# Kernel tuning notes

Hardware: AMD Instinct MI355X
Metric: run time of the kernel (lower is better)

The kernel has to match this reference:

```python
import jax, jax.numpy as jnp
import numpy as np
from jax import lax

B, S, T = 32, 64, 64
E, H = 256, 512
VS, VT = 32000, 32000


def lstm_layer(x, h0, c0, Wih, Whh, b):
    """Single-layer LSTM, batch_first. x: [B,T,in], h0/c0: [B,H].
    Gate order matches PyTorch: i, f, g, o. b = b_ih + b_hh ([4H]).
    Returns (outputs [B,T,H], hT [B,H], cT [B,H])."""
    xW = jnp.einsum('bti,gi->btg', x, Wih) + b  # precompute input projection [B,T,4H]

    def step(carry, xw_t):
        h, c = carry
        gates = xw_t + h @ Whh.T
        i, f, g, o = jnp.split(gates, 4, axis=-1)
        c = jax.nn.sigmoid(f) * c + jax.nn.sigmoid(i) * jnp.tanh(g)
        h = jax.nn.sigmoid(o) * jnp.tanh(c)
        return (h, c), h

    (hT, cT), hs = lax.scan(step, (h0, c0), jnp.swapaxes(xW, 0, 1))
    return jnp.swapaxes(hs, 0, 1), hT, cT


def setup_inputs() -> dict:
    key = jax.random.key(0)
    ks = jax.random.split(key, 24)
    w = lambda k, shape: (0.02 * jax.random.normal(k, shape)).astype(jnp.float32)
    inp = {
        'src': jax.random.randint(ks[0], (B, S), 0, VS),
        'tgt': jax.random.randint(ks[1], (B, T), 0, VT),
        'enc_emb': w(ks[2], (VS, E)),
        'dec_emb': w(ks[3], (VT, E)),
        # encoder LSTM (2 layers, unidirectional)
        'enc_Wih0': w(ks[4], (4 * H, E)),
        'enc_Whh0': w(ks[5], (4 * H, H)),
        'enc_b0': jnp.zeros((4 * H,), jnp.float32),
        'enc_Wih1': w(ks[6], (4 * H, H)),
        'enc_Whh1': w(ks[7], (4 * H, H)),
        'enc_b1': jnp.zeros((4 * H,), jnp.float32),
        # decoder LSTM (2 layers), input = embed + context -> E + H
        'dec_Wih0': w(ks[8], (4 * H, E + H)),
        'dec_Whh0': w(ks[9], (4 * H, H)),
        'dec_b0': jnp.zeros((4 * H,), jnp.float32),
        'dec_Wih1': w(ks[10], (4 * H, H)),
        'dec_Whh1': w(ks[11], (4 * H, H)),
        'dec_b1': jnp.zeros((4 * H,), jnp.float32),
        # output projection: Linear(H,H) -> tanh -> Linear(H,VT)
        'proj_W1': w(ks[12], (H, H)),
        'proj_b1': jnp.zeros((H,), jnp.float32),
        'proj_W2': w(ks[13], (VT, H)),
        'proj_b2': jnp.zeros((VT,), jnp.float32),
    }
    return inp


def reference(src, tgt, enc_emb, dec_emb,
              enc_Wih0, enc_Whh0, enc_b0, enc_Wih1, enc_Whh1, enc_b1,
              dec_Wih0, dec_Whh0, dec_b0, dec_Wih1, dec_Whh1, dec_b1,
              proj_W1, proj_b1, proj_W2, proj_b2):
    z = jnp.zeros((src.shape[0], H), jnp.float32)
    # --- encode ---
    xe = enc_emb[src]                                        # [B,S,E]
    e0, h0, c0 = lstm_layer(xe, z, z, enc_Wih0, enc_Whh0, enc_b0)
    e1, h1, c1 = lstm_layer(e0, z, z, enc_Wih1, enc_Whh1, enc_b1)
    # constant context = mean over encoder outputs (recomputed per-step in torch, hoisted here)
    context = e1.mean(axis=1)                                # [B,H]
    # --- decode with teacher forcing: input at step t is tgt[:, t] ---
    xd = dec_emb[tgt]                                        # [B,T,E]
    ctx = jnp.broadcast_to(context[:, None, :], (xd.shape[0], xd.shape[1], H))
    rnn_in = jnp.concatenate([xd, ctx], axis=-1)             # [B,T,E+H]
    d0, _, _ = lstm_layer(rnn_in, h0, c0, dec_Wih0, dec_Whh0, dec_b0)
    d1, _, _ = lstm_layer(d0, h1, c1, dec_Wih1, dec_Whh1, dec_b1)
    # --- output projection ---
    hid = jnp.tanh(d1 @ proj_W1.T + proj_b1)                 # [B,T,H]
    logits = hid @ proj_W2.T + proj_b2                       # [B,T,VT]
    return logits
```

## Files before the change

### kernel.cpp

```cpp
#include <hip/hip_runtime.h>

typedef unsigned short ushort_t;
typedef __attribute__((ext_vector_type(8))) short bf16x8;
typedef __attribute__((ext_vector_type(4))) float f32x4;

#define BB 32
#define TT 64
#define HH 512
#define G4H 2048

__device__ __forceinline__ ushort_t f2bf(float f) {
    unsigned int u = __float_as_uint(f);
    unsigned int r = (u + 0x7fffu + ((u >> 16) & 1u)) >> 16;
    return (ushort_t)r;
}
__device__ __forceinline__ float sigf(float x) { return 1.f / (1.f + __expf(-x)); }
__device__ __forceinline__ float tanh_(float x) {
    float e = __expf(2.f * x);
    return 1.f - 2.f / (e + 1.f);
}

__global__ void zero_init(float* zeros) {
    int t = threadIdx.x;
    if (t < 128) ((float4*)zeros)[t] = make_float4(0.f, 0.f, 0.f, 0.f);
}

__global__ void gather_rows(const int* __restrict__ idx, const float* __restrict__ emb,
                            float* __restrict__ out) {
    int row = blockIdx.x;
    int t = threadIdx.x;
    int id = idx[row];
    float4 v = *(const float4*)(emb + (size_t)id * 256 + t * 4);
    *(float4*)(out + (size_t)row * 256 + t * 4) = v;
}

__global__ __launch_bounds__(256) void gemm_f32(
    const float* __restrict__ A, int lda,
    const float* __restrict__ B, int ldb,
    const float* __restrict__ bias,
    void* __restrict__ Cv, int ldc,
    int M, int N, int K, int mode)
{
    __shared__ float As[16 * 68];
    __shared__ float Bs[16 * 68];
    const int tid = threadIdx.x;
    const int bm = blockIdx.y * 64, bn = blockIdx.x * 64;
    const int lr = tid >> 2, lk = (tid & 3) << 2;
    const int tr = (tid >> 4) << 2, tc = (tid & 15) << 2;
    float acc[4][4] = {};
    const int arow = bm + lr, brow = bn + lr;
    const bool aval = arow < M, bval = brow < N;
    const float* Ap = A + (size_t)arow * lda + lk;
    const float* Bp = B + (size_t)brow * ldb + lk;

    for (int k0 = 0; k0 < K; k0 += 16) {
        float4 av = make_float4(0.f, 0.f, 0.f, 0.f);
        float4 bv = make_float4(0.f, 0.f, 0.f, 0.f);
        if (aval) av = *(const float4*)(Ap + k0);
        if (bval) bv = *(const float4*)(Bp + k0);
        As[(lk + 0) * 68 + lr] = av.x; As[(lk + 1) * 68 + lr] = av.y;
        As[(lk + 2) * 68 + lr] = av.z; As[(lk + 3) * 68 + lr] = av.w;
        Bs[(lk + 0) * 68 + lr] = bv.x; Bs[(lk + 1) * 68 + lr] = bv.y;
        Bs[(lk + 2) * 68 + lr] = bv.z; Bs[(lk + 3) * 68 + lr] = bv.w;
        __syncthreads();
        #pragma unroll
        for (int kk = 0; kk < 16; kk++) {
            float4 a = *(const float4*)&As[kk * 68 + tr];
            float4 b = *(const float4*)&Bs[kk * 68 + tc];
            float ar[4] = {a.x, a.y, a.z, a.w};
            float br[4] = {b.x, b.y, b.z, b.w};
            #pragma unroll
            for (int i = 0; i < 4; i++)
                #pragma unroll
                for (int j = 0; j < 4; j++)
                    acc[i][j] = fmaf(ar[i], br[j], acc[i][j]);
        }
        __syncthreads();
    }
    #pragma unroll
    for (int i = 0; i < 4; i++) {
        int m = bm + tr + i;
        if (m >= M) continue;
        #pragma unroll
        for (int j = 0; j < 4; j++) {
            int n = bn + tc + j;
            if (n >= N) continue;
            float v = acc[i][j] + (bias ? bias[n] : 0.f);
            if (mode == 0) ((float*)Cv)[(size_t)m * ldc + n] = v;
            else ((ushort_t*)Cv)[(size_t)m * ldc + n] = f2bf(tanh_(v));
        }
    }
}

__global__ __launch_bounds__(256) void gemm_mfma(
    const float* __restrict__ A, int lda,
    const float* __restrict__ B, int ldb,
    const float* __restrict__ bias,
    void* __restrict__ Cv, int ldc, int K, int mode)
{
    __shared__ ushort_t As[128 * 72];
    __shared__ ushort_t Bs[128 * 72];
    const int tid = threadIdx.x;
    const int bm = blockIdx.x * 128, bn = blockIdx.y * 128;
    const int lane = tid & 63, wave = tid >> 6;
    const int wm = (wave & 1) * 64, wn = (wave >> 1) * 64;
    const int lr = lane & 15, lk = (lane >> 4) * 8;
    const int srow = tid >> 3, sch = tid & 7;
    f32x4 acc[4][4] = {};

    for (int k0 = 0; k0 < K; k0 += 64) {
        #pragma unroll
        for (int rr = 0; rr < 4; rr++) {
            int row = srow + rr * 32;
            const float* as = A + (size_t)(bm + row) * lda + k0 + sch * 8;
            float4 a0 = *(const float4*)as;
            float4 a1 = *(const float4*)(as + 4);
            int4 pa;
            pa.x = (int)f2bf(a0.x) | ((int)f2bf(a0.y) << 16);
            pa.y = (int)f2bf(a0.z) | ((int)f2bf(a0.w) << 16);
            pa.z = (int)f2bf(a1.x) | ((int)f2bf(a1.y) << 16);
            pa.w = (int)f2bf(a1.z) | ((int)f2bf(a1.w) << 16);
            *(int4*)&As[row * 72 + sch * 8] = pa;
            const float* bs = B + (size_t)(bn + row) * ldb + k0 + sch * 8;
            float4 f0 = *(const float4*)bs;
            float4 f1 = *(const float4*)(bs + 4);
            int4 pk;
            pk.x = (int)f2bf(f0.x) | ((int)f2bf(f0.y) << 16);
            pk.y = (int)f2bf(f0.z) | ((int)f2bf(f0.w) << 16);
            pk.z = (int)f2bf(f1.x) | ((int)f2bf(f1.y) << 16);
            pk.w = (int)f2bf(f1.z) | ((int)f2bf(f1.w) << 16);
            *(int4*)&Bs[row * 72 + sch * 8] = pk;
        }
        __syncthreads();
        #pragma unroll
        for (int k2 = 0; k2 < 64; k2 += 32) {
            bf16x8 a[4], bfr[4];
            #pragma unroll
            for (int i = 0; i < 4; i++)
                a[i] = *(const bf16x8*)&As[(wm + i * 16 + lr) * 72 + k2 + lk];
            #pragma unroll
            for (int j = 0; j < 4; j++)
                bfr[j] = *(const bf16x8*)&Bs[(wn + j * 16 + lr) * 72 + k2 + lk];
            #pragma unroll
            for (int i = 0; i < 4; i++)
                #pragma unroll
                for (int j = 0; j < 4; j++)
                    acc[i][j] = __builtin_amdgcn_mfma_f32_16x16x32_bf16(a[i], bfr[j], acc[i][j], 0, 0, 0);
        }
        __syncthreads();
    }
    const int r0 = (lane >> 4) * 4;
    #pragma unroll
    for (int j = 0; j < 4; j++) {
        int col = bn + wn + j * 16 + lr;
        float bv = bias ? bias[col] : 0.f;
        #pragma unroll
        for (int i = 0; i < 4; i++) {
            int row = bm + wm + i * 16 + r0;
            #pragma unroll
            for (int q = 0; q < 4; q++) {
                float v = acc[i][j][q] + bv;
                if (mode == 0) ((float*)Cv)[(size_t)(row + q) * ldc + col] = v;
                else ((ushort_t*)Cv)[(size_t)(row + q) * ldc + col] = f2bf(tanh_(v));
            }
        }
    }
}

__global__ void mean_ctx(const float* __restrict__ e1, float* __restrict__ ctx) {
    int g = blockIdx.x * 256 + threadIdx.x;
    int b = g >> 9, u = g & 511;
    float s = 0.f;
    #pragma unroll 8
    for (int t = 0; t < TT; t++) s += e1[((size_t)b * TT + t) * HH + u];
    ctx[g] = s * (1.f / 64.f);
}

#define LOADS16                                                            \
        "global_load_dwordx2 %0, %16, off sc0 sc1\n\t"                     \
        "global_load_dwordx2 %1, %16, off offset:256 sc0 sc1\n\t"          \
        "global_load_dwordx2 %2, %16, off offset:512 sc0 sc1\n\t"          \
        "global_load_dwordx2 %3, %16, off offset:768 sc0 sc1\n\t"          \
        "global_load_dwordx2 %4, %16, off offset:1024 sc0 sc1\n\t"         \
        "global_load_dwordx2 %5, %16, off offset:1280 sc0 sc1\n\t"         \
        "global_load_dwordx2 %6, %16, off offset:1536 sc0 sc1\n\t"         \
        "global_load_dwordx2 %7, %16, off offset:1792 sc0 sc1\n\t"         \
        "global_load_dwordx2 %8, %16, off offset:2048 sc0 sc1\n\t"         \
        "global_load_dwordx2 %9, %16, off offset:2304 sc0 sc1\n\t"         \
        "global_load_dwordx2 %10, %16, off offset:2560 sc0 sc1\n\t"        \
        "global_load_dwordx2 %11, %16, off offset:2816 sc0 sc1\n\t"        \
        "global_load_dwordx2 %12, %16, off offset:3072 sc0 sc1\n\t"        \
        "global_load_dwordx2 %13, %16, off offset:3328 sc0 sc1\n\t"        \
        "global_load_dwordx2 %14, %16, off offset:3584 sc0 sc1\n\t"        \
        "global_load_dwordx2 %15, %16, off offset:3840 sc0 sc1\n\t"

#define OUTS16(a) "=&v"(a[0]), "=&v"(a[1]), "=&v"(a[2]), "=&v"(a[3]),      \
                  "=&v"(a[4]), "=&v"(a[5]), "=&v"(a[6]), "=&v"(a[7]),      \
                  "=&v"(a[8]), "=&v"(a[9]), "=&v"(a[10]), "=&v"(a[11]),    \
                  "=&v"(a[12]), "=&v"(a[13]), "=&v"(a[14]), "=&v"(a[15])

__device__ __forceinline__ bool tag_ok16(const uint2* q, unsigned int tag) {
    unsigned int a = 0xFFFFFFFFu, o = 0u;
    #pragma unroll
    for (int i = 0; i < 16; i++) { a &= q[i].x & q[i].y; o |= q[i].x | q[i].y; }
    return ((a >> 16) == tag) & ((o >> 16) == tag);
}

__device__ __forceinline__ void poll16_f32(const uint2* rp, unsigned int tag, float* hd) {
    uint2 q[16];
    bool ok;
    do {
        asm volatile(LOADS16 "s_waitcnt vmcnt(0)"
                     : OUTS16(q) : "v"(rp) : "memory");
        __builtin_amdgcn_sched_barrier(0);
        ok = tag_ok16(q, tag);
    } while (!ok);
    #pragma unroll
    for (int i = 0; i < 16; i++)
        hd[32 * i] = __uint_as_float((q[i].x << 16) | (q[i].y & 0xFFFFu));
}
__device__ __forceinline__ void poll16_bf16(const uint2* rp, unsigned int tag, ushort_t* hd) {
    uint2 q[16];
    bool ok;
    do {
        asm volatile(LOADS16 "s_waitcnt vmcnt(0)"
                     : OUTS16(q) : "v"(rp) : "memory");
        __builtin_amdgcn_sched_barrier(0);
        ok = tag_ok16(q, tag);
    } while (!ok);
    #pragma unroll
    for (int i = 0; i < 16; i++)
        hd[32 * i] = f2bf(__uint_as_float((q[i].x << 16) | (q[i].y & 0xFFFFu)));
}
__device__ __forceinline__ void poll_dual(const uint2* rp1, unsigned int tag1, float* hd,
                                          const uint2* rp0, unsigned int tag0, ushort_t* ad) {
    uint2 q[16], r[16];
    bool ok;
    do {
        asm volatile(LOADS16 : OUTS16(q) : "v"(rp1) : "memory");
        asm volatile(LOADS16 "s_waitcnt vmcnt(0)"
                     : OUTS16(r) : "v"(rp0) : "memory");
        __builtin_amdgcn_sched_barrier(0);
        ok = tag_ok16(q, tag1) & tag_ok16(r, tag0);
    } while (!ok);
    #pragma unroll
    for (int i = 0; i < 16; i++) {
        hd[32 * i] = __uint_as_float((q[i].x << 16) | (q[i].y & 0xFFFFu));
        ad[32 * i] = f2bf(__uint_as_float((r[i].x << 16) | (r[i].y & 0xFFFFu)));
    }
}

__global__ __launch_bounds__(512) void scan_pair2(
    const float* __restrict__ gatesX0,
    const float* __restrict__ ctxAdd0,
    const float* __restrict__ Whh0,
    const float* __restrict__ Wih1,
    const float* __restrict__ Whh1,
    const float* __restrict__ b1,
    const float* __restrict__ h00, int sh00, const float* __restrict__ c00, int sc00,
    const float* __restrict__ h01, int sh01, const float* __restrict__ c01, int sc01,
    float* __restrict__ out0, float* __restrict__ out1,
    float* __restrict__ cT0o, float* __restrict__ cT1o,
    uint2* __restrict__ ring0, uint2* __restrict__ ring1,
    int tb0, int tb1)
{
    __shared__ float wlds[32 * 516];
    __shared__ float hmain[16 * 516];
    __shared__ float glds[16 * 36];
    __shared__ ushort_t ah[16 * 520];
    __shared__ float pglds[8 * 256];
    const int tid = threadIdx.x;
    const bool isL1 = blockIdx.x >= 128;
    const int rb = blockIdx.x & 127;
    const int bg = rb >> 6, ub = rb & 63, u0 = ub * 8;
    const int w = tid >> 6, l = tid & 63;
    const int bb = l >> 2, rr = w * 4 + (l & 3);
    const int grow = (rr >> 3) * HH + u0 + (rr & 7);
    const int batch = bg * 16 + bb;
    const int srow = tid >> 5, hc0 = tid & 31;

    {
        const float* W = isL1 ? Whh1 : Whh0;
        const int sr = tid >> 4, ch = (tid & 15) * 32;
        const float* ws = W + (size_t)((sr >> 3) * HH + u0 + (sr & 7)) * HH + ch;
        float* wd = &wlds[sr * 516 + ch];
        #pragma unroll
        for (int j = 0; j < 32; j += 4) *(f32x4*)(wd + j) = *(const f32x4*)(ws + j);
    }
    const int ni = w & 1, kh = w >> 1, lr = l & 15, ls = l >> 4;
    bf16x8 bfrag[4];
    if (isL1) {
        const int nrow = ni * 16 + lr;
        const int gN = (nrow >> 3) * HH + u0 + (nrow & 7);
        const float* wr = Wih1 + (size_t)gN * HH + kh * 128 + ls * 8;
        #pragma unroll
        for (int kk = 0; kk < 4; kk++) {
            float f[8];
            *(f32x4*)&f[0] = *(const f32x4*)(wr + kk * 32);
            *(f32x4*)&f[4] = *(const f32x4*)(wr + kk * 32 + 4);
            bf16x8 hv;
            #pragma unroll
            for (int j = 0; j < 8; j++) hv[j] = (short)f2bf(f[j]);
            bfrag[kk] = hv;
        }
    }
    {
        const float* hsrc = isL1 ? h01 : h00;
        const int hstr = isL1 ? sh01 : sh00;
        const float* hs = hsrc + (size_t)(bg * 16 + srow) * hstr;
        float* hd = &hmain[srow * 516 + hc0];
        #pragma unroll
        for (int j = 0; j < 16; j++) hd[32 * j] = hs[hc0 + 32 * j];
    }
    const int pb = tid >> 3, pu = tid & 7, gbatch = bg * 16 + pb;
    float creg = 0.f, b1v0 = 0.f, b1v1 = 0.f, b1v2 = 0.f, b1v3 = 0.f;
    if (tid < 128) {
        const float* ci = isL1 ? c01 : c00;
        const int cs = isL1 ? sc01 : sc00;
        creg = ci[(size_t)gbatch * cs + u0 + pu];
        if (isL1) {
            b1v0 = b1[0 * HH + u0 + pu]; b1v1 = b1[1 * HH + u0 + pu];
            b1v2 = b1[2 * HH + u0 + pu]; b1v3 = b1[3 * HH + u0 + pu];
        }
    }
    float xctx = 0.f, gx_cur = 0.f, gx_nxt = 0.f;
    const float* gxp = nullptr;
    if (!isL1) {
        gxp = gatesX0 + (size_t)batch * TT * G4H + grow;
        gx_cur = gxp[0];
        if (ctxAdd0) xctx = ctxAdd0[(size_t)batch * G4H + grow];
    } else {
        const uint2* rp = ring0 + ((size_t)0 * BB + bg * 16 + srow) * HH + hc0;
        poll16_bf16(rp, (unsigned int)(tb0 + 1), &ah[srow * 520 + hc0]);
    }
    float* outp = isL1 ? out1 : out0;
    uint2* ringp = isL1 ? ring1 : ring0;
    const int tbase = isL1 ? tb1 : tb0;

    for (int t = 0; t < TT; ++t) {
        __syncthreads();
        if (!isL1) {
            int tn = (t + 1 < TT) ? t + 1 : t;
            gx_nxt = gxp[(size_t)tn * G4H];
            f32x4 s = {0.f, 0.f, 0.f, 0.f};
            const float* hp = &hmain[bb * 516];
            const float* wp = &wlds[rr * 516];
            #pragma unroll 8
            for (int k = 0; k < HH; k += 4) {
                f32x4 hv = *(const f32x4*)(hp + k);
                f32x4 wv = *(const f32x4*)(wp + k);
                s.x = fmaf(hv.x, wv.x, s.x); s.y = fmaf(hv.y, wv.y, s.y);
                s.z = fmaf(hv.z, wv.z, s.z); s.w = fmaf(hv.w, wv.w, s.w);
            }
            glds[bb * 36 + rr] = gx_cur + xctx + ((s.x + s.y) + (s.z + s.w));
        } else {
            f32x4 acc = {0.f, 0.f, 0.f, 0.f};
            const ushort_t* ab = &ah[lr * 520 + kh * 128 + ls * 8];
            #pragma unroll
            for (int kk = 0; kk < 4; kk++) {
                bf16x8 av = *(const bf16x8*)(ab + kk * 32);
                acc = __builtin_amdgcn_mfma_f32_16x16x32_bf16(av, bfrag[kk], acc, 0, 0, 0);
            }
            #pragma unroll
            for (int q = 0; q < 4; q++)
                pglds[(kh * 2 + ni) * 256 + (ls * 4 + q) * 16 + lr] = acc[q];
            f32x4 s = {0.f, 0.f, 0.f, 0.f};
            const float* hp = &hmain[bb * 516];
            const float* wp = &wlds[rr * 516];
            #pragma unroll 8
            for (int k = 0; k < HH; k += 4) {
                f32x4 hv = *(const f32x4*)(hp + k);
                f32x4 wv = *(const f32x4*)(wp + k);
                s.x = fmaf(hv.x, wv.x, s.x); s.y = fmaf(hv.y, wv.y, s.y);
                s.z = fmaf(hv.z, wv.z, s.z); s.w = fmaf(hv.w, wv.w, s.w);
            }
            glds[bb * 36 + rr] = (s.x + s.y) + (s.z + s.w);
        }
        __syncthreads();
        const unsigned int tag = (unsigned int)(tbase + t + 1);
        if (tid < 128) {
            float pre[4];
            if (!isL1) {
                #pragma unroll
                for (int g = 0; g < 4; g++) pre[g] = glds[pb * 36 + g * 8 + pu];
            } else {
                float bv[4] = {b1v0, b1v1, b1v2, b1v3};
                #pragma unroll
                for (int g = 0; g < 4; g++) {
                    int r = g * 8 + pu;
                    int nit = r >> 4, cr = r & 15;
                    float p = glds[pb * 36 + r] + bv[g];
                    #pragma unroll
                    for (int k2 = 0; k2 < 4; k2++)
                        p += pglds[(k2 * 2 + nit) * 256 + pb * 16 + cr];
                    pre[g] = p;
                }
            }
            float c = sigf(pre[1]) * creg + sigf(pre[0]) * tanh_(pre[2]);
            float h = sigf(pre[3]) * tanh_(c);
            creg = c;
            outp[((size_t)gbatch * TT + t) * HH + u0 + pu] = h;
            unsigned int hu = __float_as_uint(h);
            uint2 wv2;
            wv2.x = (tag << 16) | (hu >> 16);
            wv2.y = (tag << 16) | (hu & 0xFFFFu);
            uint2* pp = ringp + ((size_t)t * BB + gbatch) * HH + u0 + pu;
            asm volatile("global_store_dwordx2 %0, %1, off sc0 sc1"
                         :: "v"(pp), "v"(wv2) : "memory");
            if (t == TT - 1) {
                if (!isL1 && cT0o) cT0o[(size_t)gbatch * HH + u0 + pu] = c;
                if (isL1 && cT1o)  cT1o[(size_t)gbatch * HH + u0 + pu] = c;
            }
        }
        if (t + 1 < TT) {
            if (!isL1) {
                const uint2* rp = ring0 + ((size_t)t * BB + bg * 16 + srow) * HH + hc0;
                poll16_f32(rp, tag, &hmain[srow * 516 + hc0]);
            } else {
                const uint2* rp1 = ring1 + ((size_t)t * BB + bg * 16 + srow) * HH + hc0;
                const uint2* rp0 = ring0 + ((size_t)(t + 1) * BB + bg * 16 + srow) * HH + hc0;
                poll_dual(rp1, tag, &hmain[srow * 516 + hc0],
                          rp0, (unsigned int)(tb0 + t + 2), &ah[srow * 520 + hc0]);
            }
        }
        gx_cur = gx_nxt;
    }
}

__global__ __launch_bounds__(256) void gemm_bf16(
    const ushort_t* __restrict__ A,
    const float* __restrict__ B,
    const float* __restrict__ bias,
    float* __restrict__ C, int M, int N, int K)
{
    __shared__ ushort_t As[128 * 72];
    __shared__ ushort_t Bs[128 * 72];
    const int tid = threadIdx.x;
    const int bm = blockIdx.x * 128, bn = blockIdx.y * 128;
    const int lane = tid & 63, wave = tid >> 6;
    const int wm = (wave & 1) * 64, wn = (wave >> 1) * 64;
    const int lr = lane & 15, lk = (lane >> 4) * 8;
    const int srow = tid >> 3, sch = tid & 7;
    f32x4 acc[4][4] = {};

    for (int k0 = 0; k0 < K; k0 += 64) {
        #pragma unroll
        for (int rr = 0; rr < 4; rr++) {
            int row = srow + rr * 32;
            const ushort_t* as = A + (size_t)(bm + row) * K + k0 + sch * 8;
            *(int4*)&As[row * 72 + sch * 8] = *(const int4*)as;
            const float* bs = B + (size_t)(bn + row) * K + k0 + sch * 8;
            float4 f0 = *(const float4*)bs;
            float4 f1 = *(const float4*)(bs + 4);
            int4 pk;
            pk.x = (int)f2bf(f0.x) | ((int)f2bf(f0.y) << 16);
            pk.y = (int)f2bf(f0.z) | ((int)f2bf(f0.w) << 16);
            pk.z = (int)f2bf(f1.x) | ((int)f2bf(f1.y) << 16);
            pk.w = (int)f2bf(f1.z) | ((int)f2bf(f1.w) << 16);
            *(int4*)&Bs[row * 72 + sch * 8] = pk;
        }
        __syncthreads();
        #pragma unroll
        for (int k2 = 0; k2 < 64; k2 += 32) {
            bf16x8 a[4], bfr[4];
            #pragma unroll
            for (int i = 0; i < 4; i++)
                a[i] = *(const bf16x8*)&As[(wm + i * 16 + lr) * 72 + k2 + lk];
            #pragma unroll
            for (int j = 0; j < 4; j++)
                bfr[j] = *(const bf16x8*)&Bs[(wn + j * 16 + lr) * 72 + k2 + lk];
            #pragma unroll
            for (int i = 0; i < 4; i++)
                #pragma unroll
                for (int j = 0; j < 4; j++)
                    acc[i][j] = __builtin_amdgcn_mfma_f32_16x16x32_bf16(a[i], bfr[j], acc[i][j], 0, 0, 0);
        }
        __syncthreads();
    }
    const int r0 = (lane >> 4) * 4;
    #pragma unroll
    for (int j = 0; j < 4; j++) {
        int col = bn + wn + j * 16 + lr;
        float bv = bias[col];
        #pragma unroll
        for (int i = 0; i < 4; i++) {
            int row = bm + wm + i * 16 + r0;
            #pragma unroll
            for (int q = 0; q < 4; q++)
                C[(size_t)(row + q) * N + col] = acc[i][j][q] + bv;
        }
    }
}

extern "C" void kernel_launch(void* const* d_in, const int* in_sizes, int n_in,
                              void* d_out, int out_size, void* d_ws, size_t ws_size,
                              hipStream_t stream) {
    const int*   src      = (const int*)d_in[0];
    const int*   tgt      = (const int*)d_in[1];
    const float* enc_emb  = (const float*)d_in[2];
    const float* dec_emb  = (const float*)d_in[3];
    const float* eWih0    = (const float*)d_in[4];
    const float* eWhh0    = (const float*)d_in[5];
    const float* eb0      = (const float*)d_in[6];
    const float* eWih1    = (const float*)d_in[7];
    const float* eWhh1    = (const float*)d_in[8];
    const float* eb1      = (const float*)d_in[9];
    const float* dWih0    = (const float*)d_in[10];
    const float* dWhh0    = (const float*)d_in[11];
    const float* db0      = (const float*)d_in[12];
    const float* dWih1    = (const float*)d_in[13];
    const float* dWhh1    = (const float*)d_in[14];
    const float* db1      = (const float*)d_in[15];
    const float* pW1      = (const float*)d_in[16];
    const float* pb1      = (const float*)d_in[17];
    const float* pW2      = (const float*)d_in[18];
    const float* pb2      = (const float*)d_in[19];
    float* out = (float*)d_out;

    float* fws   = (float*)d_ws;
    float* zeros = fws;
    float* cT0   = fws + 2048;
    float* cT1   = cT0 + 16384;
    float* ctx   = cT1 + 16384;
    float* ctxW  = ctx + 16384;
    ushort_t* hid = (ushort_t*)(ctxW + 65536);

    float* G0  = out;
    float* G1  = G0 + 4194304;
    float* G2  = G1 + 4194304;
    float* G3  = G2 + 4194304;
    float* xe  = G3 + 4194304;
    float* xd  = xe + 524288;
    float* e0  = xd + 524288;
    float* e1  = e0 + 1048576;
    float* d0  = e1 + 1048576;
    float* d1v = d0 + 1048576;
    uint2* ring0 = (uint2*)(d1v + 1048576);
    uint2* ring1 = ring0 + 1048576;

    zero_init<<<1, 256, 0, stream>>>(zeros);
    gather_rows<<<2048, 64, 0, stream>>>(src, enc_emb, xe);
    gather_rows<<<2048, 64, 0, stream>>>(tgt, dec_emb, xd);

    gemm_mfma<<<dim3(16, 16), 256, 0, stream>>>(xe, 256, eWih0, 256, eb0, G0, 2048, 256, 0);
    gemm_mfma<<<dim3(16, 16), 256, 0, stream>>>(xd, 256, dWih0, 768, db0, G2, 2048, 256, 0);

    scan_pair2<<<256, 512, 0, stream>>>(
        G0, nullptr, eWhh0, eWih1, eWhh1, eb1,
        zeros, 0, zeros, 0, zeros, 0, zeros, 0,
        e0, e1, cT0, cT1, ring0, ring1, 0, 64);

    mean_ctx<<<64, 256, 0, stream>>>(e1, ctx);
    gemm_f32<<<dim3(32, 1), 256, 0, stream>>>(ctx, 512, dWih0 + 256, 768, nullptr, ctxW, 2048, 32, 2048, 512, 0);

    scan_pair2<<<256, 512, 0, stream>>>(
        G2, ctxW, dWhh0, dWih1, dWhh1, db1,
        e0 + 63 * 512, 64 * 512, cT0, 512,
        e1 + 63 * 512, 64 * 512, cT1, 512,
        d0, d1v, nullptr, nullptr, ring0, ring1, 128, 192);

    gemm_mfma<<<dim3(16, 4), 256, 0, stream>>>(d1v, 512, pW1, 512, pb1, hid, 512, 512, 2);
    gemm_bf16<<<dim3(16, 250), 256, 0, stream>>>(hid, pW2, pb2, out, 2048, 32000, 512);
}
```

Baseline: 1.737 ms.

## Compute layer-1 recurrent matmul with split-bf16 MFMA instead of fp32 FMA

In the layer-1 scan blocks, the fp32 h·Whh1 dot-product loop is replaced by bf16 MFMA using a hi/lo split of both h and Whh1 (three MFMAs per k-slice), folded into the same accumulator as the Wih1 projection. Whh1 fragments now live in registers rather than LDS, and the hidden state is stored as hi/lo bf16 arrays. The aim is to shorten the serial per-step recurrent compute on the critical path. The cost is extra MFMAs, register pressure and split conversions, and the ring polling changes from one combined dual poll to two sequential polls.

```diff
diff --git a/kernel.cpp b/kernel.cpp
--- a/kernel.cpp
+++ b/kernel.cpp
@@ -13,6 +13,12 @@
     unsigned int u = __float_as_uint(f);
     unsigned int r = (u + 0x7fffu + ((u >> 16) & 1u)) >> 16;
     return (ushort_t)r;
+}
+__device__ __forceinline__ void split_bf(float f, ushort_t& hi, ushort_t& lo) {
+    unsigned int hu = f2bf(f);
+    hi = (ushort_t)hu;
+    float hf = __uint_as_float((unsigned int)hu << 16);
+    lo = f2bf(f - hf);
 }
 __device__ __forceinline__ float sigf(float x) { return 1.f / (1.f + __expf(-x)); }
 __device__ __forceinline__ float tanh_(float x) {
@@ -232,21 +238,21 @@
     for (int i = 0; i < 16; i++)
         hd[32 * i] = f2bf(__uint_as_float((q[i].x << 16) | (q[i].y & 0xFFFFu)));
 }
-__device__ __forceinline__ void poll_dual(const uint2* rp1, unsigned int tag1, float* hd,
-                                          const uint2* rp0, unsigned int tag0, ushort_t* ad) {
-    uint2 q[16], r[16];
+__device__ __forceinline__ void poll16_hilo(const uint2* rp, unsigned int tag,
+                                            ushort_t* hh, ushort_t* hl) {
+    uint2 q[16];
     bool ok;
     do {
-        asm volatile(LOADS16 : OUTS16(q) : "v"(rp1) : "memory");
         asm volatile(LOADS16 "s_waitcnt vmcnt(0)"
-                     : OUTS16(r) : "v"(rp0) : "memory");
+                     : OUTS16(q) : "v"(rp) : "memory");
         __builtin_amdgcn_sched_barrier(0);
-        ok = tag_ok16(q, tag1) & tag_ok16(r, tag0);
+        ok = tag_ok16(q, tag);
     } while (!ok);
     #pragma unroll
     for (int i = 0; i < 16; i++) {
-        hd[32 * i] = __uint_as_float((q[i].x << 16) | (q[i].y & 0xFFFFu));
-        ad[32 * i] = f2bf(__uint_as_float((r[i].x << 16) | (r[i].y & 0xFFFFu)));
+        float v = __uint_as_float((q[i].x << 16) | (q[i].y & 0xFFFFu));
+        ushort_t hi, lo; split_bf(v, hi, lo);
+        hh[32 * i] = hi; hl[32 * i] = lo;
     }
 }
 
@@ -268,6 +274,8 @@
     __shared__ float hmain[16 * 516];
     __shared__ float glds[16 * 36];
     __shared__ ushort_t ah[16 * 520];
+    __shared__ ushort_t ahh[16 * 520];
+    __shared__ ushort_t ahl[16 * 520];
     __shared__ float pglds[8 * 256];
     const int tid = threadIdx.x;
     const bool isL1 = blockIdx.x >= 128;
@@ -279,20 +287,20 @@
     const int batch = bg * 16 + bb;
     const int srow = tid >> 5, hc0 = tid & 31;
 
-    {
-        const float* W = isL1 ? Whh1 : Whh0;
+    if (!isL1) {
         const int sr = tid >> 4, ch = (tid & 15) * 32;
-        const float* ws = W + (size_t)((sr >> 3) * HH + u0 + (sr & 7)) * HH + ch;
+        const float* ws = Whh0 + (size_t)((sr >> 3) * HH + u0 + (sr & 7)) * HH + ch;
         float* wd = &wlds[sr * 516 + ch];
         #pragma unroll
         for (int j = 0; j < 32; j += 4) *(f32x4*)(wd + j) = *(const f32x4*)(ws + j);
     }
     const int ni = w & 1, kh = w >> 1, lr = l & 15, ls = l >> 4;
-    bf16x8 bfrag[4];
+    bf16x8 bfrag[4], wh_hi[4], wh_lo[4];
     if (isL1) {
         const int nrow = ni * 16 + lr;
         const int gN = (nrow >> 3) * HH + u0 + (nrow & 7);
         const float* wr = Wih1 + (size_t)gN * HH + kh * 128 + ls * 8;
+        const float* wr2 = Whh1 + (size_t)gN * HH + kh * 128 + ls * 8;
         #pragma unroll
         for (int kk = 0; kk < 4; kk++) {
             float f[8];
@@ -302,15 +310,33 @@
             #pragma unroll
             for (int j = 0; j < 8; j++) hv[j] = (short)f2bf(f[j]);
             bfrag[kk] = hv;
+            *(f32x4*)&f[0] = *(const f32x4*)(wr2 + kk * 32);
+            *(f32x4*)&f[4] = *(const f32x4*)(wr2 + kk * 32 + 4);
+            bf16x8 hv2, lv2;
+            #pragma unroll
+            for (int j = 0; j < 8; j++) {
+                ushort_t hu2, lu2; split_bf(f[j], hu2, lu2);
+                hv2[j] = (short)hu2; lv2[j] = (short)lu2;
+            }
+            wh_hi[kk] = hv2; wh_lo[kk] = lv2;
         }
     }
     {
-        const float* hsrc = isL1 ? h01 : h00;
-        const int hstr = isL1 ? sh01 : sh00;
-        const float* hs = hsrc + (size_t)(bg * 16 + srow) * hstr;
-        float* hd = &hmain[srow * 516 + hc0];
-        #pragma unroll
-        for (int j = 0; j < 16; j++) hd[32 * j] = hs[hc0 + 32 * j];
+        if (!isL1) {
+            const float* hs = h00 + (size_t)(bg * 16 + srow) * sh00;
+            float* hd = &hmain[srow * 516 + hc0];
+            #pragma unroll
+            for (int j = 0; j < 16; j++) hd[32 * j] = hs[hc0 + 32 * j];
+        } else {
+            const float* hs = h01 + (size_t)(bg * 16 + srow) * sh01;
+            ushort_t* hh = &ahh[srow * 520 + hc0];
+            ushort_t* hl = &ahl[srow * 520 + hc0];
+            #pragma unroll
+            for (int j = 0; j < 16; j++) {
+                ushort_t hi2, lo2; split_bf(hs[hc0 + 32 * j], hi2, lo2);
+                hh[32 * j] = hi2; hl[32 * j] = lo2;
+            }
+        }
     }
     const int pb = tid >> 3, pu = tid & 7, gbatch = bg * 16 + pb;
     float creg = 0.f, b1v0 = 0.f, b1v1 = 0.f, b1v2 = 0.f, b1v3 = 0.f;
@@ -355,26 +381,23 @@
             glds[bb * 36 + rr] = gx_cur + xctx + ((s.x + s.y) + (s.z + s.w));
         } else {
             f32x4 acc = {0.f, 0.f, 0.f, 0.f};
-            const ushort_t* ab = &ah[lr * 520 + kh * 128 + ls * 8];
+            const int abase = lr * 520 + kh * 128 + ls * 8;
+            const ushort_t* ab  = &ah[abase];
+            const ushort_t* abh = &ahh[abase];
+            const ushort_t* abl = &ahl[abase];
             #pragma unroll
             for (int kk = 0; kk < 4; kk++) {
                 bf16x8 av = *(const bf16x8*)(ab + kk * 32);
                 acc = __builtin_amdgcn_mfma_f32_16x16x32_bf16(av, bfrag[kk], acc, 0, 0, 0);
+                bf16x8 hhv = *(const bf16x8*)(abh + kk * 32);
+                bf16x8 hlv = *(const bf16x8*)(abl + kk * 32);
+                acc = __builtin_amdgcn_mfma_f32_16x16x32_bf16(hhv, wh_hi[kk], acc, 0, 0, 0);
+                acc = __builtin_amdgcn_mfma_f32_16x16x32_bf16(hlv, wh_hi[kk], acc, 0, 0, 0);
+                acc = __builtin_amdgcn_mfma_f32_16x16x32_bf16(hhv, wh_lo[kk], acc, 0, 0, 0);
             }
             #pragma unroll
             for (int q = 0; q < 4; q++)
                 pglds[(kh * 2 + ni) * 256 + (ls * 4 + q) * 16 + lr] = acc[q];
-            f32x4 s = {0.f, 0.f, 0.f, 0.f};
-            const float* hp = &hmain[bb * 516];
-            const float* wp = &wlds[rr * 516];
-            #pragma unroll 8
-            for (int k = 0; k < HH; k += 4) {
-                f32x4 hv = *(const f32x4*)(hp + k);
-                f32x4 wv = *(const f32x4*)(wp + k);
-                s.x = fmaf(hv.x, wv.x, s.x); s.y = fmaf(hv.y, wv.y, s.y);
-                s.z = fmaf(hv.z, wv.z, s.z); s.w = fmaf(hv.w, wv.w, s.w);
-            }
-            glds[bb * 36 + rr] = (s.x + s.y) + (s.z + s.w);
         }
         __syncthreads();
         const unsigned int tag = (unsigned int)(tbase + t + 1);
@@ -389,7 +412,7 @@
                 for (int g = 0; g < 4; g++) {
                     int r = g * 8 + pu;
                     int nit = r >> 4, cr = r & 15;
-                    float p = glds[pb * 36 + r] + bv[g];
+                    float p = bv[g];
                     #pragma unroll
                     for (int k2 = 0; k2 < 4; k2++)
                         p += pglds[(k2 * 2 + nit) * 256 + pb * 16 + cr];
@@ -418,9 +441,9 @@
                 poll16_f32(rp, tag, &hmain[srow * 516 + hc0]);
             } else {
                 const uint2* rp1 = ring1 + ((size_t)t * BB + bg * 16 + srow) * HH + hc0;
+                poll16_hilo(rp1, tag, &ahh[srow * 520 + hc0], &ahl[srow * 520 + hc0]);
                 const uint2* rp0 = ring0 + ((size_t)(t + 1) * BB + bg * 16 + srow) * HH + hc0;
-                poll_dual(rp1, tag, &hmain[srow * 516 + hc0],
-                          rp0, (unsigned int)(tb0 + t + 2), &ah[srow * 520 + hc0]);
+                poll16_bf16(rp0, (unsigned int)(tb0 + t + 2), &ah[srow * 520 + hc0]);
             }
         }
         gx_cur = gx_nxt;
```

New measurement: 1.443 ms. 1.2x faster.
